# Kernel optimization log

Hardware: AMD Instinct MI355X
Metric: run time of the kernel (lower is better)

## Reference

```python
import jax, jax.numpy as jnp
import numpy as np
import math

M = 0.2
S = 30.0
COS_M = math.cos(M)
SIN_M = math.sin(M)
TH = math.cos(math.pi - M)
MM = math.sin(math.pi - M) * M


def setup_inputs() -> dict:
    key = jax.random.key(0)
    k1, k2, k3 = jax.random.split(key, 3)
    B, D, C = 1024, 192, 100000
    x = jax.random.normal(k1, (B, D), dtype=jnp.float32)
    weight = jax.random.normal(k2, (C, D), dtype=jnp.float32)
    label = jax.random.randint(k3, (B,), 0, C, dtype=jnp.int64)
    return {"x": x, "weight": weight, "label": label}


def _l2norm(v, axis=-1, eps=1e-12):
    # matches F.normalize(p=2): v / max(||v||, eps)
    n = jnp.sqrt(jnp.sum(v * v, axis=axis, keepdims=True))
    return v / jnp.maximum(n, eps)


def reference(x, weight, label):
    B = x.shape[0]
    cosine = _l2norm(x) @ _l2norm(weight).T            # [B, C]
    sine = jnp.sqrt(jnp.clip(1.0 - cosine * cosine, 0.0, 1.0))
    phi = cosine * COS_M - sine * SIN_M
    phi = jnp.where(cosine - TH > 0, phi, cosine - MM)
    one_hot = jax.nn.one_hot(label, cosine.shape[1], dtype=cosine.dtype)
    output = (one_hot * phi + (1.0 - one_hot) * cosine) * S
    # cross entropy (mean reduction)
    logp = jax.nn.log_softmax(output, axis=-1)
    loss = -jnp.mean(jnp.take_along_axis(logp, label[:, None], axis=1)[:, 0])
    # top-1 accuracy (percent), detached metric
    pred = jnp.argmax(output, axis=-1)
    prec1 = jnp.mean((pred == label).astype(jnp.float32)) * 100.0
    return loss, prec1
```

## Files before the change

### kernel.cpp

```cpp
#include <hip/hip_runtime.h>
#include <math.h>

#define B_ROWS   1024
#define DIM      192
#define NCLS     100000
#define S_SCALE  30.0f
#define COS_M    0.98006657784124163f
#define SIN_M    0.19866933079506122f
#define TH_C     (-0.98006657784124163f)
#define MM_C     0.039733866159012243f
#define L2E30    43.2808512266689f

#define NTILE_B  784
#define NCHUNKR  16
#define ASEG_CH  1536
#define NSLOT    1568

#define NCHUNKC  1568
#define CSPLIT   64
#define NSLOT2   64
#define PACK_WGRID 3136
#define PACK_GRID  3168

typedef float floatx4 __attribute__((ext_vector_type(4)));
typedef __bf16 bf16x8 __attribute__((ext_vector_type(8)));

__device__ __forceinline__ unsigned int f2bf(float x) {
    unsigned int u = __float_as_uint(x);
    u = (u + 0x7fffu + ((u >> 16) & 1u)) >> 16;
    return u;
}
__device__ __forceinline__ unsigned int pack2(float lo, float hi) {
    return f2bf(lo) | (f2bf(hi) << 16);
}
__device__ __forceinline__ float fexp2(float x) {
#if __has_builtin(__builtin_amdgcn_exp2f)
    return __builtin_amdgcn_exp2f(x);
#else
    float r; __asm__("v_exp_f32 %0, %1" : "=v"(r) : "v"(x)); return r;
#endif
}
template <int N>
__device__ __forceinline__ float ror16(float x) {
    return __int_as_float(__builtin_amdgcn_mov_dpp(
        __float_as_int(x), 0x120 | N, 0xF, 0xF, false));
}


__global__ __launch_bounds__(256)
void pack_kernel(const float* __restrict__ x, const float* __restrict__ w,
                 unsigned short* __restrict__ asw, unsigned short* __restrict__ wsw,
                 float* __restrict__ accum)
{
    const int bid = blockIdx.x;
    const int t = threadIdx.x;
    const int r = t >> 3, oct = t & 7;

    const float* src;
    unsigned short* dst;
    int row;
    bool live;
    if (bid < PACK_WGRID) {
        row = bid * 32 + r;  live = (row < NCLS);  src = w;  dst = wsw;
    } else {
        row = (bid - PACK_WGRID) * 32 + r;  live = true;  src = x;  dst = asw;
        if (bid == PACK_WGRID && t < 4) accum[t] = 0.0f;
    }

    float4 buf[6];
    float s = 0.f;
    if (live) {
        const float4* sp = (const float4*)(src + (size_t)row * DIM) + oct * 6;
        #pragma unroll
        for (int q = 0; q < 6; ++q) {
            float4 v = sp[q];
            buf[q] = v;
            s += v.x * v.x + v.y * v.y + v.z * v.z + v.w * v.w;
        }
    } else {
        #pragma unroll
        for (int q = 0; q < 6; ++q) buf[q] = make_float4(0.f, 0.f, 0.f, 0.f);
    }
    s += __shfl_xor(s, 1);
    s += __shfl_xor(s, 2);
    s += __shfl_xor(s, 4);
    const float inv = live ? (1.0f / fmaxf(sqrtf(s), 1e-12f)) : 0.0f;

    const int cc = row >> 6, c64 = row & 63;
    #pragma unroll
    for (int j = 0; j < 3; ++j) {
        const int k8 = oct * 3 + j;
        uint4 o;
        float4 a0 = buf[2 * j], a1 = buf[2 * j + 1];
        o.x = pack2(a0.x * inv, a0.y * inv);
        o.y = pack2(a0.z * inv, a0.w * inv);
        o.z = pack2(a1.x * inv, a1.y * inv);
        o.w = pack2(a1.z * inv, a1.w * inv);
        *(uint4*)(dst + ((size_t)(cc * 24 + k8) * 64 + c64) * 8) = o;
    }
}

__global__ __launch_bounds__(256, 4)
void gemm_stats2_kernel(const unsigned short* __restrict__ asw,
                        const unsigned short* __restrict__ wsw,
                        float2* __restrict__ pslot)
{
    const int bid  = blockIdx.x;
    const int cs   = (bid & 7) * 8 + ((bid >> 3) & 7);
    const int rt   = bid >> 6;
    const int tid  = threadIdx.x;
    const int wv   = tid >> 6;
    const int lane = tid & 63;
    const int quad = lane >> 4, mrow = lane & 15;

    bf16x8 xfr[6];
    {
        const unsigned short* ab = asw + (size_t)rt * (ASEG_CH * 8);
        #pragma unroll
        for (int ks = 0; ks < 6; ++ks)
            xfr[ks] = *(const bf16x8*)(ab +
                (size_t)((ks * 4 + quad) * 64 + wv * 16 + mrow) * 8);
    }

    const int nch = 24 + ((cs & 1) ? 0 : 1);
    const unsigned short* wp = wsw
        + (size_t)(cs * 24 + ((cs + 1) >> 1)) * 12288
        + quad * 512 + mrow * 8;

    float s_acc[4] = {0.f, 0.f, 0.f, 0.f};
    float m_acc[4] = {-1e30f, -1e30f, -1e30f, -1e30f};

    bf16x8 c0 = *(const bf16x8*)(wp);
    bf16x8 c1 = *(const bf16x8*)(wp + 128);
    bf16x8 c2 = *(const bf16x8*)(wp + 256);
    bf16x8 c3 = *(const bf16x8*)(wp + 384);

    #pragma unroll 1
    for (int c = 0; c < nch; ++c, wp += 12288) {
        floatx4 acc0 = {0.f, 0.f, 0.f, 0.f};
        floatx4 acc1 = {0.f, 0.f, 0.f, 0.f};
        floatx4 acc2 = {0.f, 0.f, 0.f, 0.f};
        floatx4 acc3 = {0.f, 0.f, 0.f, 0.f};
        #pragma unroll
        for (int ks = 0; ks < 6; ++ks) {
            const unsigned short* np = (ks < 5) ? (wp + (ks + 1) * 2048)
                                                : (wp + 12288);
            bf16x8 n0 = *(const bf16x8*)(np);
            bf16x8 n1 = *(const bf16x8*)(np + 128);
            bf16x8 n2 = *(const bf16x8*)(np + 256);
            bf16x8 n3 = *(const bf16x8*)(np + 384);
            acc0 = __builtin_amdgcn_mfma_f32_16x16x32_bf16(xfr[ks], c0, acc0, 0, 0, 0);
            acc1 = __builtin_amdgcn_mfma_f32_16x16x32_bf16(xfr[ks], c1, acc1, 0, 0, 0);
            acc2 = __builtin_amdgcn_mfma_f32_16x16x32_bf16(xfr[ks], c2, acc2, 0, 0, 0);
            acc3 = __builtin_amdgcn_mfma_f32_16x16x32_bf16(xfr[ks], c3, acc3, 0, 0, 0);
            c0 = n0; c1 = n1; c2 = n2; c3 = n3;
        }
        #pragma unroll
        for (int r = 0; r < 4; ++r) {
            float v0 = acc0[r], v1 = acc1[r], v2 = acc2[r], v3 = acc3[r];
            m_acc[r] = fmaxf(m_acc[r], fmaxf(fmaxf(v0, v1), fmaxf(v2, v3)));
            s_acc[r] += (fexp2(fmaf(v0, L2E30, -L2E30))
                       + fexp2(fmaf(v1, L2E30, -L2E30)))
                      + (fexp2(fmaf(v2, L2E30, -L2E30))
                       + fexp2(fmaf(v3, L2E30, -L2E30)));
        }
    }

    const int rowb = rt * 64 + wv * 16 + quad * 4;
    #pragma unroll
    for (int r = 0; r < 4; ++r) {
        float s = s_acc[r], m = m_acc[r];
        s += ror16<1>(s); s += ror16<2>(s); s += ror16<4>(s); s += ror16<8>(s);
        m = fmaxf(m, ror16<1>(m)); m = fmaxf(m, ror16<2>(m));
        m = fmaxf(m, ror16<4>(m)); m = fmaxf(m, ror16<8>(m));
        if (mrow == 0)
            pslot[(size_t)cs * B_ROWS + rowb + r] = make_float2(m, s);
    }
}

__global__ __launch_bounds__(256)
void finalize2_kernel(const float2* __restrict__ pslot,
                      const float* __restrict__ x, const float* __restrict__ w,
                      const int* __restrict__ label,
                      float* __restrict__ accum, float* __restrict__ out)
{
    __shared__ float2 red[8][32];
    const int t = threadIdx.x, rr = t & 31, g = t >> 5;
    {
        const int row = blockIdx.x * 32 + rr;
        float M = -1e30f, L = 0.f;
        #pragma unroll
        for (int s = 0; s < NSLOT2 / 8; ++s) {
            float2 p = pslot[(size_t)(s * 8 + g) * B_ROWS + row];
            M = fmaxf(M, p.x);
            L += p.y;
        }
        red[g][rr] = make_float2(M, L);
    }
    __syncthreads();
    if (t < 32) {
        const int row = blockIdx.x * 32 + t;
        float Mc = -1e30f, L = 0.f;
        #pragma unroll
        for (int g2 = 0; g2 < 8; ++g2) {
            float2 p = red[g2][t];
            Mc = fmaxf(Mc, p.x);
            L += p.y;
        }

        const int lab = label[row];
        const float4* xr = (const float4*)(x + (size_t)row * DIM);
        const float4* wr = (const float4*)(w + (size_t)lab * DIM);
        float dot = 0.f, nx = 0.f, nw = 0.f;
        #pragma unroll
        for (int q = 0; q < 48; ++q) {
            float4 a = xr[q], b = wr[q];
            dot += a.x * b.x + a.y * b.y + a.z * b.z + a.w * b.w;
            nx  += a.x * a.x + a.y * a.y + a.z * a.z + a.w * a.w;
            nw  += b.x * b.x + b.y * b.y + b.z * b.z + b.w * b.w;
        }
        float cosl    = dot / fmaxf(sqrtf(nx) * sqrtf(nw), 1e-12f);
        float t_plain = S_SCALE * cosl;
        float sine    = sqrtf(fmaxf(0.f, fminf(1.f, 1.f - cosl * cosl)));
        float phi     = cosl * COS_M - sine * SIN_M;
        float modv    = ((cosl - TH_C) > 0.f) ? phi : (cosl - MM_C);
        float t_mod   = S_SCALE * modv;

        float Ladj = L - __expf(t_plain - 30.0f) + __expf(t_mod - 30.0f);
        Ladj = fmaxf(Ladj, 1e-37f);
        float loss = (30.0f + logf(Ladj)) - t_mod;
        float corr = (t_mod > S_SCALE * Mc) ? 1.f : 0.f;

        #pragma unroll
        for (int off = 16; off > 0; off >>= 1) {
            loss += __shfl_xor(loss, off);
            corr += __shfl_xor(corr, off);
        }
        if (t == 0) {
            atomicAdd(&accum[0], loss);
            atomicAdd(&accum[1], corr);
            __threadfence();
            int old = atomicAdd((int*)accum + 2, 1);
            if (old == (int)gridDim.x - 1) {
                float a0 = atomicAdd(&accum[0], 0.0f);
                float a1 = atomicAdd(&accum[1], 0.0f);
                out[0] = a0 * (1.0f / (float)B_ROWS);
                out[1] = a1 * (100.0f / (float)B_ROWS);
            }
        }
    }
}


__global__ __launch_bounds__(256)
void prep_kernel(const float* __restrict__ x, unsigned short* __restrict__ asw,
                 float* __restrict__ accum)
{
    const int ab = blockIdx.x;
    const int t = threadIdx.x;
    if (ab == 0 && t < 4) accum[t] = 0.0f;
    const int r = t >> 1, half = t & 1;
    const int row = ab * 128 + r;
    const int c = ab * 2 + (r >> 6);
    const int r64 = r & 63;

    float4 buf[24];
    float s = 0.f;
    const float4* sp = (const float4*)(x + (size_t)row * DIM) + half * 24;
    #pragma unroll
    for (int q = 0; q < 24; ++q) {
        float4 v = sp[q];
        buf[q] = v;
        s += v.x * v.x + v.y * v.y + v.z * v.z + v.w * v.w;
    }
    s += __shfl_xor(s, 1);
    const float inv = 1.0f / fmaxf(sqrtf(s), 1e-12f);
    #pragma unroll
    for (int j = 0; j < 12; ++j) {
        const int k8 = half * 12 + j;
        uint4 o;
        float4 a0 = buf[2 * j], a1 = buf[2 * j + 1];
        o.x = pack2(a0.x * inv, a0.y * inv);
        o.y = pack2(a0.z * inv, a0.w * inv);
        o.z = pack2(a1.x * inv, a1.y * inv);
        o.w = pack2(a1.z * inv, a1.w * inv);
        *(uint4*)(asw + ((size_t)c * ASEG_CH + k8 * 64 + r64) * 8) = o;
    }
}

__global__ __launch_bounds__(256, 3)
void gemm_stats_kernel(const float* __restrict__ w,
                       const unsigned short* __restrict__ asw,
                       unsigned int* __restrict__ pslot)
{
    __shared__ __align__(16) char lds[49152];
    const int tid  = threadIdx.x;
    const int wave = tid >> 6;
    const int lane = tid & 63;
    const int quad = lane >> 4;
    const int mrow = lane & 15;
    const int rg   = wave >> 1;
    const int cgr  = wave & 1;

    {
        const int r = tid >> 1, half = tid & 1;
        const int col = blockIdx.x * 128 + r;
        const bool live = (col < NCLS);
        float4 buf[24];
        float s = 0.f;
        if (live) {
            const float4* sp = (const float4*)(w + (size_t)col * DIM) + half * 24;
            #pragma unroll
            for (int q = 0; q < 24; ++q) {
                float4 v = sp[q];
                buf[q] = v;
                s += v.x * v.x + v.y * v.y + v.z * v.z + v.w * v.w;
            }
        }
        s += __shfl_xor(s, 1);
        const float inv = live ? (1.0f / fmaxf(sqrtf(s), 1e-12f)) : 0.0f;
        #pragma unroll
        for (int j = 0; j < 12; ++j) {
            const int k8 = half * 12 + j;
            uint4 o = make_uint4(0u, 0u, 0u, 0u);
            if (live) {
                float4 a0 = buf[2 * j], a1 = buf[2 * j + 1];
                o.x = pack2(a0.x * inv, a0.y * inv);
                o.y = pack2(a0.z * inv, a0.w * inv);
                o.z = pack2(a1.x * inv, a1.y * inv);
                o.w = pack2(a1.z * inv, a1.w * inv);
            }
            *(uint4*)(lds + (size_t)(k8 * 128 + r) * 16) = o;
        }
    }
    __syncthreads();

    bf16x8 bfr[6][4];
    #pragma unroll
    for (int ks = 0; ks < 6; ++ks)
        #pragma unroll
        for (int ni = 0; ni < 4; ++ni)
            bfr[ks][ni] = *(const bf16x8*)(lds +
                (((ks * 4 + quad) * 128) + cgr * 64 + ni * 16 + mrow) * 16);

    const int slot = blockIdx.x * 2 + cgr;
    #pragma unroll 2
    for (int c = 0; c < NCHUNKR; ++c) {
        const unsigned short* ab = asw + (size_t)c * ASEG_CH * 8;
        floatx4 acc[2][4];
        #pragma unroll
        for (int mi = 0; mi < 2; ++mi)
            #pragma unroll
            for (int ni = 0; ni < 4; ++ni) {
                floatx4 z = {0.f, 0.f, 0.f, 0.f};
                acc[mi][ni] = z;
            }
        #pragma unroll
        for (int ks = 0; ks < 6; ++ks) {
            bf16x8 a0 = *(const bf16x8*)(ab +
                (size_t)(((ks * 4 + quad) * 64) + rg * 32 + mrow) * 8);
            bf16x8 a1 = *(const bf16x8*)(ab +
                (size_t)(((ks * 4 + quad) * 64) + rg * 32 + 16 + mrow) * 8);
            #pragma unroll
            for (int ni = 0; ni < 4; ++ni)
                acc[0][ni] = __builtin_amdgcn_mfma_f32_16x16x32_bf16(
                    a0, bfr[ks][ni], acc[0][ni], 0, 0, 0);
            #pragma unroll
            for (int ni = 0; ni < 4; ++ni)
                acc[1][ni] = __builtin_amdgcn_mfma_f32_16x16x32_bf16(
                    a1, bfr[ks][ni], acc[1][ni], 0, 0, 0);
        }

        #pragma unroll
        for (int mi = 0; mi < 2; ++mi)
            #pragma unroll
            for (int r = 0; r < 4; ++r) {
                float v0 = acc[mi][0][r], v1 = acc[mi][1][r];
                float v2 = acc[mi][2][r], v3 = acc[mi][3][r];
                float m = fmaxf(fmaxf(v0, v1), fmaxf(v2, v3));
                float s = fexp2(fmaf(v0, L2E30, -L2E30))
                        + fexp2(fmaf(v1, L2E30, -L2E30))
                        + fexp2(fmaf(v2, L2E30, -L2E30))
                        + fexp2(fmaf(v3, L2E30, -L2E30));
                s += ror16<1>(s); s += ror16<2>(s);
                s += ror16<4>(s); s += ror16<8>(s);
                m = fmaxf(m, ror16<1>(m)); m = fmaxf(m, ror16<2>(m));
                m = fmaxf(m, ror16<4>(m)); m = fmaxf(m, ror16<8>(m));
                if (mrow == mi * 4 + r)
                    pslot[(size_t)slot * B_ROWS +
                          c * 64 + rg * 32 + mi * 16 + quad * 4 + r] = pack2(m, s);
            }
    }
}

__global__ __launch_bounds__(256)
void finalize_kernel(const unsigned int* __restrict__ pslot,
                     const float* __restrict__ x, const float* __restrict__ w,
                     const int* __restrict__ label,
                     float* __restrict__ accum, float* __restrict__ out)
{
    __shared__ float2 red[8][32];
    const int t = threadIdx.x, rr = t & 31, g = t >> 5;
    {
        const int row = blockIdx.x * 32 + rr;
        float M = -1e30f, L = 0.f;
        for (int s = g; s < NSLOT; s += 8) {
            unsigned int u = pslot[(size_t)s * B_ROWS + row];
            M = fmaxf(M, __uint_as_float(u << 16));
            L += __uint_as_float(u & 0xFFFF0000u);
        }
        red[g][rr] = make_float2(M, L);
    }
    __syncthreads();
    if (t < 32) {
        const int row = blockIdx.x * 32 + t;
        float Mc = -1e30f, L = 0.f;
        #pragma unroll
        for (int g2 = 0; g2 < 8; ++g2) {
            float2 p = red[g2][t];
            Mc = fmaxf(Mc, p.x);
            L += p.y;
        }

        const int lab = label[row];
        const float4* xr = (const float4*)(x + (size_t)row * DIM);
        const float4* wr = (const float4*)(w + (size_t)lab * DIM);
        float dot = 0.f, nx = 0.f, nw = 0.f;
        #pragma unroll
        for (int q = 0; q < 48; ++q) {
            float4 a = xr[q], b = wr[q];
            dot += a.x * b.x + a.y * b.y + a.z * b.z + a.w * b.w;
            nx  += a.x * a.x + a.y * a.y + a.z * a.z + a.w * a.w;
            nw  += b.x * b.x + b.y * b.y + b.z * b.z + b.w * b.w;
        }
        float cosl    = dot / fmaxf(sqrtf(nx) * sqrtf(nw), 1e-12f);
        float t_plain = S_SCALE * cosl;
        float sine    = sqrtf(fmaxf(0.f, fminf(1.f, 1.f - cosl * cosl)));
        float phi     = cosl * COS_M - sine * SIN_M;
        float modv    = ((cosl - TH_C) > 0.f) ? phi : (cosl - MM_C);
        float t_mod   = S_SCALE * modv;

        float Ladj = L - __expf(t_plain - 30.0f) + __expf(t_mod - 30.0f);
        Ladj = fmaxf(Ladj, 1e-37f);
        float loss = (30.0f + logf(Ladj)) - t_mod;
        float corr = (t_mod > S_SCALE * Mc) ? 1.f : 0.f;

        #pragma unroll
        for (int off = 16; off > 0; off >>= 1) {
            loss += __shfl_xor(loss, off);
            corr += __shfl_xor(corr, off);
        }
        if (t == 0) {
            atomicAdd(&accum[0], loss);
            atomicAdd(&accum[1], corr);
            __threadfence();
            int old = atomicAdd((int*)accum + 2, 1);
            if (old == (int)gridDim.x - 1) {
                float a0 = atomicAdd(&accum[0], 0.0f);
                float a1 = atomicAdd(&accum[1], 0.0f);
                out[0] = a0 * (1.0f / (float)B_ROWS);
                out[1] = a1 * (100.0f / (float)B_ROWS);
            }
        }
    }
}

extern "C" void kernel_launch(void* const* d_in, const int* in_sizes, int n_in,
                              void* d_out, int out_size, void* d_ws, size_t ws_size,
                              hipStream_t stream)
{
    const float* x     = (const float*)d_in[0];
    const float* w     = (const float*)d_in[1];
    const int*   label = (const int*)d_in[2];
    float* out = (float*)d_out;

    char* ws = (char*)d_ws;
    float* accum = (float*)ws;
    unsigned short* asw = (unsigned short*)(ws + 256);
    const size_t asw_bytes = (size_t)NCHUNKR * ASEG_CH * 16;

    const size_t wsw_bytes   = (size_t)NCHUNKC * 24 * 64 * 16;
    const size_t pslot2_bytes = (size_t)NSLOT2 * B_ROWS * 8;
    const size_t need_new = 256 + asw_bytes + wsw_bytes + pslot2_bytes;

    if (ws_size >= need_new) {
        unsigned short* wsw = (unsigned short*)(ws + 256 + asw_bytes);
        float2* pslot2 = (float2*)(ws + 256 + asw_bytes + wsw_bytes);
        pack_kernel<<<dim3(PACK_GRID), dim3(256), 0, stream>>>(x, w, asw, wsw, accum);
        gemm_stats2_kernel<<<dim3(1024), dim3(256), 0, stream>>>(asw, wsw, pslot2);
        finalize2_kernel<<<dim3(B_ROWS / 32), dim3(256), 0, stream>>>(
            pslot2, x, w, label, accum, out);
    } else {
        unsigned int* pslot = (unsigned int*)(ws + 256 + asw_bytes);
        prep_kernel<<<dim3(8), dim3(256), 0, stream>>>(x, asw, accum);
        gemm_stats_kernel<<<dim3(NTILE_B), dim3(256), 0, stream>>>(w, asw, pslot);
        finalize_kernel<<<dim3(B_ROWS / 32), dim3(256), 0, stream>>>(
            pslot, x, w, label, accum, out);
    }
}
```

Baseline: 197.8 us.

## Enlarge GEMM row tile to 64 rows per wave for weight reuse

Restructures the fused GEMM+softmax-stats kernel so each wave holds four 16-row A fragments and reuses every loaded weight fragment across 64 batch rows instead of 16. The class dimension is split into 128 slices and the grid drops from 1024 to 512 blocks, with occupancy lowered to 2 blocks per SM. This cuts global and L2 traffic for weights by four, at the cost of many more registers (16 accumulators plus 24 A fragments) and fewer resident waves to hide latency.

```diff
diff --git a/kernel.cpp b/kernel.cpp
--- a/kernel.cpp
+++ b/kernel.cpp
@@ -17,8 +17,8 @@
 #define NSLOT    1568
 
 #define NCHUNKC  1568
-#define CSPLIT   64
-#define NSLOT2   64
+#define CSPLIT   128
+#define NSLOT2   128
 #define PACK_WGRID 3136
 #define PACK_GRID  3168
 
@@ -100,35 +100,41 @@
     }
 }
 
-__global__ __launch_bounds__(256, 4)
-void gemm_stats2_kernel(const unsigned short* __restrict__ asw,
+__global__ __launch_bounds__(256, 2)
+void gemm_stats3_kernel(const unsigned short* __restrict__ asw,
                         const unsigned short* __restrict__ wsw,
                         float2* __restrict__ pslot)
 {
     const int bid  = blockIdx.x;
-    const int cs   = (bid & 7) * 8 + ((bid >> 3) & 7);
-    const int rt   = bid >> 6;
+    const int cs   = bid & 127;
+    const int rb   = bid >> 7;
     const int tid  = threadIdx.x;
     const int wv   = tid >> 6;
     const int lane = tid & 63;
     const int quad = lane >> 4, mrow = lane & 15;
 
-    bf16x8 xfr[6];
+    bf16x8 xfr[4][6];
     {
-        const unsigned short* ab = asw + (size_t)rt * (ASEG_CH * 8);
-        #pragma unroll
-        for (int ks = 0; ks < 6; ++ks)
-            xfr[ks] = *(const bf16x8*)(ab +
-                (size_t)((ks * 4 + quad) * 64 + wv * 16 + mrow) * 8);
-    }
-
-    const int nch = 24 + ((cs & 1) ? 0 : 1);
-    const unsigned short* wp = wsw
-        + (size_t)(cs * 24 + ((cs + 1) >> 1)) * 12288
-        + quad * 512 + mrow * 8;
-
-    float s_acc[4] = {0.f, 0.f, 0.f, 0.f};
-    float m_acc[4] = {-1e30f, -1e30f, -1e30f, -1e30f};
+        const unsigned short* ab = asw + (size_t)(rb * 4 + wv) * (24 * 64 * 8);
+        #pragma unroll
+        for (int a = 0; a < 4; ++a)
+            #pragma unroll
+            for (int ks = 0; ks < 6; ++ks)
+                xfr[a][ks] = *(const bf16x8*)(ab +
+                    (size_t)((ks * 4 + quad) * 64 + a * 16 + mrow) * 8);
+    }
+
+    const int nch   = 12 + (cs < 32 ? 1 : 0);
+    const int cbase = cs * 12 + (cs < 32 ? cs : 32);
+    const unsigned short* wp = wsw + (size_t)cbase * 12288
+                             + quad * 512 + mrow * 8;
+
+    float s_acc[4][4];
+    float m_acc[4][4];
+    #pragma unroll
+    for (int a = 0; a < 4; ++a)
+        #pragma unroll
+        for (int r = 0; r < 4; ++r) { s_acc[a][r] = 0.f; m_acc[a][r] = -1e30f; }
 
     bf16x8 c0 = *(const bf16x8*)(wp);
     bf16x8 c1 = *(const bf16x8*)(wp + 128);
@@ -137,10 +143,14 @@
 
     #pragma unroll 1
     for (int c = 0; c < nch; ++c, wp += 12288) {
-        floatx4 acc0 = {0.f, 0.f, 0.f, 0.f};
-        floatx4 acc1 = {0.f, 0.f, 0.f, 0.f};
-        floatx4 acc2 = {0.f, 0.f, 0.f, 0.f};
-        floatx4 acc3 = {0.f, 0.f, 0.f, 0.f};
+        floatx4 acc[4][4];
+        #pragma unroll
+        for (int a = 0; a < 4; ++a)
+            #pragma unroll
+            for (int ni = 0; ni < 4; ++ni) {
+                floatx4 z = {0.f, 0.f, 0.f, 0.f};
+                acc[a][ni] = z;
+            }
         #pragma unroll
         for (int ks = 0; ks < 6; ++ks) {
             const unsigned short* np = (ks < 5) ? (wp + (ks + 1) * 2048)
@@ -149,33 +159,47 @@
             bf16x8 n1 = *(const bf16x8*)(np + 128);
             bf16x8 n2 = *(const bf16x8*)(np + 256);
             bf16x8 n3 = *(const bf16x8*)(np + 384);
-            acc0 = __builtin_amdgcn_mfma_f32_16x16x32_bf16(xfr[ks], c0, acc0, 0, 0, 0);
-            acc1 = __builtin_amdgcn_mfma_f32_16x16x32_bf16(xfr[ks], c1, acc1, 0, 0, 0);
-            acc2 = __builtin_amdgcn_mfma_f32_16x16x32_bf16(xfr[ks], c2, acc2, 0, 0, 0);
-            acc3 = __builtin_amdgcn_mfma_f32_16x16x32_bf16(xfr[ks], c3, acc3, 0, 0, 0);
+            #pragma unroll
+            for (int a = 0; a < 4; ++a) {
+                acc[a][0] = __builtin_amdgcn_mfma_f32_16x16x32_bf16(
+                    xfr[a][ks], c0, acc[a][0], 0, 0, 0);
+                acc[a][1] = __builtin_amdgcn_mfma_f32_16x16x32_bf16(
+                    xfr[a][ks], c1, acc[a][1], 0, 0, 0);
+                acc[a][2] = __builtin_amdgcn_mfma_f32_16x16x32_bf16(
+                    xfr[a][ks], c2, acc[a][2], 0, 0, 0);
+                acc[a][3] = __builtin_amdgcn_mfma_f32_16x16x32_bf16(
+                    xfr[a][ks], c3, acc[a][3], 0, 0, 0);
+            }
             c0 = n0; c1 = n1; c2 = n2; c3 = n3;
         }
         #pragma unroll
+        for (int a = 0; a < 4; ++a)
+            #pragma unroll
+            for (int r = 0; r < 4; ++r) {
+                float v0 = acc[a][0][r], v1 = acc[a][1][r];
+                float v2 = acc[a][2][r], v3 = acc[a][3][r];
+                m_acc[a][r] = fmaxf(m_acc[a][r],
+                                    fmaxf(fmaxf(v0, v1), fmaxf(v2, v3)));
+                s_acc[a][r] += (fexp2(fmaf(v0, L2E30, -L2E30))
+                              + fexp2(fmaf(v1, L2E30, -L2E30)))
+                             + (fexp2(fmaf(v2, L2E30, -L2E30))
+                              + fexp2(fmaf(v3, L2E30, -L2E30)));
+            }
+    }
+
+    const int rowb = rb * 256 + wv * 64;
+    #pragma unroll
+    for (int a = 0; a < 4; ++a)
+        #pragma unroll
         for (int r = 0; r < 4; ++r) {
-            float v0 = acc0[r], v1 = acc1[r], v2 = acc2[r], v3 = acc3[r];
-            m_acc[r] = fmaxf(m_acc[r], fmaxf(fmaxf(v0, v1), fmaxf(v2, v3)));
-            s_acc[r] += (fexp2(fmaf(v0, L2E30, -L2E30))
-                       + fexp2(fmaf(v1, L2E30, -L2E30)))
-                      + (fexp2(fmaf(v2, L2E30, -L2E30))
-                       + fexp2(fmaf(v3, L2E30, -L2E30)));
-        }
-    }
-
-    const int rowb = rt * 64 + wv * 16 + quad * 4;
-    #pragma unroll
-    for (int r = 0; r < 4; ++r) {
-        float s = s_acc[r], m = m_acc[r];
-        s += ror16<1>(s); s += ror16<2>(s); s += ror16<4>(s); s += ror16<8>(s);
-        m = fmaxf(m, ror16<1>(m)); m = fmaxf(m, ror16<2>(m));
-        m = fmaxf(m, ror16<4>(m)); m = fmaxf(m, ror16<8>(m));
-        if (mrow == 0)
-            pslot[(size_t)cs * B_ROWS + rowb + r] = make_float2(m, s);
-    }
+            float s = s_acc[a][r], m = m_acc[a][r];
+            s += ror16<1>(s); s += ror16<2>(s); s += ror16<4>(s); s += ror16<8>(s);
+            m = fmaxf(m, ror16<1>(m)); m = fmaxf(m, ror16<2>(m));
+            m = fmaxf(m, ror16<4>(m)); m = fmaxf(m, ror16<8>(m));
+            if (mrow == 0)
+                pslot[(size_t)cs * B_ROWS + rowb + a * 16 + quad * 4 + r] =
+                    make_float2(m, s);
+        }
 }
 
 __global__ __launch_bounds__(256)
@@ -479,7 +503,7 @@
     unsigned short* asw = (unsigned short*)(ws + 256);
     const size_t asw_bytes = (size_t)NCHUNKR * ASEG_CH * 16;
 
-    const size_t wsw_bytes   = (size_t)NCHUNKC * 24 * 64 * 16;
+    const size_t wsw_bytes    = (size_t)NCHUNKC * 24 * 64 * 16;
     const size_t pslot2_bytes = (size_t)NSLOT2 * B_ROWS * 8;
     const size_t need_new = 256 + asw_bytes + wsw_bytes + pslot2_bytes;
 
@@ -487,7 +511,7 @@
         unsigned short* wsw = (unsigned short*)(ws + 256 + asw_bytes);
         float2* pslot2 = (float2*)(ws + 256 + asw_bytes + wsw_bytes);
         pack_kernel<<<dim3(PACK_GRID), dim3(256), 0, stream>>>(x, w, asw, wsw, accum);
-        gemm_stats2_kernel<<<dim3(1024), dim3(256), 0, stream>>>(asw, wsw, pslot2);
+        gemm_stats3_kernel<<<dim3(4 * CSPLIT), dim3(256), 0, stream>>>(asw, wsw, pslot2);
         finalize2_kernel<<<dim3(B_ROWS / 32), dim3(256), 0, stream>>>(
             pslot2, x, w, label, accum, out);
     } else {
```

After: 162.5 us. -17.9%, faster.
